# Kernel tuning notes

Measured on AMD Instinct MI355X. Metric: run time of the kernel, lower is better.

Reference implementation:

```python
import jax, jax.numpy as jnp
import numpy as np

BATCH, SEQ, H, P, HID, CHUNK = 2, 2048, 32, 64, 2048, 256
NORM_EPS = 1e-5


def setup_inputs() -> dict:
    key = jax.random.key(0)
    ks = jax.random.split(key, 10)
    f = lambda k, sh, sc=1.0: jax.random.normal(k, sh, jnp.float32) * sc
    return {
        "hidden_states_ab": f(ks[0], (BATCH, SEQ, HID), 0.02),
        "hidden_states_g": f(ks[1], (BATCH, SEQ, HID), 0.02),
        "q_states": f(ks[2], (BATCH, SEQ, H, P)),
        "k_states": f(ks[3], (BATCH, SEQ, H, P)),
        "v_states": f(ks[4], (BATCH, SEQ, H, P)),
        "dt_w": f(ks[5], (HID, H), 0.02),
        "dt_b": jnp.zeros((H,), jnp.float32),
        "g_w": f(ks[6], (HID, H), 0.02),
        "g_b": jnp.zeros((H,), jnp.float32),
        "A_log": jnp.log(jnp.arange(1, H + 1, dtype=jnp.float32)),
        "dt_bias": jnp.ones((H,), jnp.float32),
        "norm_weight": jnp.ones((H * P,), jnp.float32),
        "o_w": f(ks[7], (H, P, P), 0.02),
        "o_b": jnp.zeros((H, P), jnp.float32),
    }


def _l2norm(x, eps=1e-12):
    # torch F.normalize(p=2, dim=-1): x / max(||x||, eps)
    n = jnp.sqrt(jnp.sum(x * x, axis=-1, keepdims=True))
    return x / jnp.maximum(n, eps)


def _ssd(x, dt, A, Bm, Cm, chunk):
    # x: (b,s,h,p)  dt: (b,s,h) post-softplus  A: (h,)  Bm/Cm: (b,s,h,n)
    b, s, h, p = x.shape
    n = Bm.shape[-1]
    c = s // chunk
    rs = lambda t: t.reshape(b, c, chunk, *t.shape[2:])
    x, dt, Bm, Cm = rs(x), rs(dt), rs(Bm), rs(Cm)
    a = dt * A                         # (b,c,L,h) log-decay increments
    cum = jnp.cumsum(a, axis=2)        # (b,c,L,h)
    cumT = jnp.swapaxes(cum, 2, 3)     # (b,c,h,L)
    # intra-chunk (quadratic, causal) part
    diff = cumT[..., :, None] - cumT[..., None, :]          # (b,c,h,L,L)
    mask = jnp.tril(jnp.ones((chunk, chunk), bool))
    decay = jnp.exp(jnp.where(mask, diff, -jnp.inf))
    CB = jnp.einsum('bclhn,bcshn->bchls', Cm, Bm)
    scores = CB * decay * jnp.swapaxes(dt, 2, 3)[:, :, :, None, :]
    y = jnp.einsum('bchls,bcshp->bclhp', scores, x)
    # per-chunk states
    decay_last = jnp.exp(cumT[..., -1:] - cumT)             # (b,c,h,L)
    w = jnp.swapaxes(decay_last, 2, 3) * dt                 # (b,c,L,h)
    states = jnp.einsum('bclh,bclhn,bclhp->bchpn', w, Bm, x)
    # inter-chunk recurrence over c chunks
    chunk_decay = jnp.exp(cumT[..., -1])                    # (b,c,h)
    def step(Hs, inp):
        cd, st = inp
        return cd[..., None, None] * Hs + st, Hs
    H_last, H_prev = jax.lax.scan(
        step, jnp.zeros((b, h, p, n), x.dtype),
        (jnp.moveaxis(chunk_decay, 1, 0), jnp.moveaxis(states, 1, 0)))
    H_prev = jnp.moveaxis(H_prev, 0, 1)                     # (b,c,h,p,n)
    y = y + jnp.einsum('bclhn,bclh,bchpn->bclhp', Cm, jnp.exp(cum), H_prev)
    return y.reshape(b, s, h, p), H_last


def reference(hidden_states_ab, hidden_states_g, q_states, k_states, v_states,
              dt_w, dt_b, g_w, g_b, A_log, dt_bias, norm_weight, o_w, o_b):
    b, s, h, p = v_states.shape
    Cm = _l2norm(q_states)
    Bm = _l2norm(k_states)
    # dt_proj bias + mamba dt_bias, then softplus (dt_softplus=True)
    dt = jax.nn.softplus(hidden_states_ab @ dt_w + dt_b + dt_bias)   # (b,s,h)
    A = -jnp.exp(A_log)
    y, ssm_state = _ssd(v_states, dt, A, Bm, Cm, CHUNK)
    # gate: g_proj then repeat_interleave(head_dim) on last dim
    gate = jnp.repeat(hidden_states_g @ g_w + g_b, p, axis=-1)       # (b,s,h*p)
    # RMSNormGated, norm_before_gate=False: normalize(x * silu(z)) * weight
    y = y.reshape(b, s, h * p) * jax.nn.silu(gate)
    y = y * jax.lax.rsqrt(jnp.mean(y * y, axis=-1, keepdims=True) + NORM_EPS)
    y = y * norm_weight
    # GroupLinear o_proj: per-head (p -> p) linear
    out = jnp.einsum('bshp,hpq->bshq', y.reshape(b, s, h, p), o_w) + o_b
    return out.reshape(b, s, h * p)
```

## Files before the change

kernel.cpp:

```cpp
#include <hip/hip_runtime.h>
#include <math.h>

#define BATCH 2
#define SEQ   2048
#define NH    32
#define HID   2048
#define CHUNK 256
#define NCH   8
#define NBCH  (BATCH*NCH*NH)
#define PST   72
#define BK    256
#define APST  264
#define KSPLIT 4
#define KSEG  (HID / KSPLIT)

typedef __attribute__((ext_vector_type(4))) float f32x4;
typedef __attribute__((ext_vector_type(8))) short bf16x8;
typedef unsigned int uint;
typedef unsigned short ushort;

__device__ __forceinline__ float softplusf(float x) {
    return x > 20.f ? x : log1pf(expf(x));
}

__device__ __forceinline__ short f2bf(float f) {
    union { float f; uint u; } v; v.f = f;
    uint r = v.u + 0x7FFF + ((v.u >> 16) & 1);
    return (short)(r >> 16);
}
__device__ __forceinline__ float bf2f(ushort s) {
    union { uint u; float f; } v; v.u = ((uint)s) << 16; return v.f;
}
__device__ __forceinline__ uint packbf2(float lo, float hi) {
    return (uint)(ushort)f2bf(lo) | ((uint)(ushort)f2bf(hi) << 16);
}

struct BF8 { union { bf16x8 v; short s[8]; }; };

__device__ __forceinline__ bf16x8 load_cvt8(const float* p, float scale) {
    float4 a = *(const float4*)p;
    float4 b = *(const float4*)(p + 4);
    BF8 r;
    r.s[0]=f2bf(a.x*scale); r.s[1]=f2bf(a.y*scale); r.s[2]=f2bf(a.z*scale); r.s[3]=f2bf(a.w*scale);
    r.s[4]=f2bf(b.x*scale); r.s[5]=f2bf(b.y*scale); r.s[6]=f2bf(b.z*scale); r.s[7]=f2bf(b.w*scale);
    return r.v;
}

__device__ __forceinline__ bf16x8 cvt8(float4 a, float4 b, float s) {
    BF8 r;
    r.s[0]=f2bf(a.x*s); r.s[1]=f2bf(a.y*s); r.s[2]=f2bf(a.z*s); r.s[3]=f2bf(a.w*s);
    r.s[4]=f2bf(b.x*s); r.s[5]=f2bf(b.y*s); r.s[6]=f2bf(b.z*s); r.s[7]=f2bf(b.w*s);
    return r.v;
}

#define MFMA(a,b,c) __builtin_amdgcn_mfma_f32_16x16x32_bf16((a),(b),(c),0,0,0)

__global__ __launch_bounds__(256) void k_proj(
    const float* __restrict__ hs_ab, const float* __restrict__ hs_g,
    const float* __restrict__ dt_w, const float* __restrict__ g_w,
    const float* __restrict__ o_w,  const float* __restrict__ norm_w,
    float* __restrict__ part, short* __restrict__ nwWT)
{
    __shared__ __align__(16) short As[32 * APST];
    __shared__ __align__(16) short Bs[32 * APST];
    int blk = blockIdx.x;
    int t = threadIdx.x;

    if (blk >= 2 * KSPLIT * 128) {
        int h = blk - 2 * KSPLIT * 128;
        float* tile = (float*)As;
        {
            int p = t >> 2, q0 = (t & 3) * 16;
            const float* wp = o_w + (size_t)h * 4096 + p * 64 + q0;
            #pragma unroll
            for (int i = 0; i < 4; ++i)
                *(float4*)(tile + p * 64 + q0 + i * 4) = *(const float4*)(wp + i * 4);
        }
        __syncthreads();
        int q = t >> 2, p0 = (t & 3) * 16;
        uint us[8];
        #pragma unroll
        for (int j = 0; j < 8; ++j) {
            float lo = tile[(p0 + 2*j    ) * 64 + q] * norm_w[h * 64 + p0 + 2*j];
            float hi = tile[(p0 + 2*j + 1) * 64 + q] * norm_w[h * 64 + p0 + 2*j + 1];
            us[j] = packbf2(lo, hi);
        }
        uint* dst = (uint*)(nwWT + (size_t)h * 4096 + q * 64 + p0);
        *(uint4*)dst       = make_uint4(us[0], us[1], us[2], us[3]);
        *(uint4*)(dst + 4) = make_uint4(us[4], us[5], us[6], us[7]);
        return;
    }

    int ksp = blk >> 8;
    int rem = blk & 255;
    int which = rem >> 7;
    int rt = rem & 127;
    int r0 = rt * 32;
    const float* Am = which ? hs_g : hs_ab;
    const float* W  = which ? g_w  : dt_w;
    int w = t >> 6, lane = t & 63, quad = lane >> 4, l16 = lane & 15;
    int mh = w & 1, nh = w >> 1;

    f32x4 acc = (f32x4){0.f, 0.f, 0.f, 0.f};

    for (int kc = ksp * KSEG; kc < ksp * KSEG + KSEG; kc += BK) {
        __syncthreads();
        {
            int row = t >> 3, k0 = (t & 7) * 32;
            const float* src = Am + (size_t)(r0 + row) * HID + kc + k0;
            uint* dst = (uint*)(As + row * APST + k0);
            #pragma unroll
            for (int i = 0; i < 4; ++i) {
                float4 a = *(const float4*)(src + i * 8);
                float4 b = *(const float4*)(src + i * 8 + 4);
                dst[i*4+0] = packbf2(a.x, a.y); dst[i*4+1] = packbf2(a.z, a.w);
                dst[i*4+2] = packbf2(b.x, b.y); dst[i*4+3] = packbf2(b.z, b.w);
            }
        }
        if (t < 128) {
            int k2 = t * 2;
            const float* w0 = W + (size_t)(kc + k2) * NH;
            const float* w1 = w0 + NH;
            #pragma unroll
            for (int n = 0; n < 32; n += 4) {
                float4 a = *(const float4*)(w0 + n);
                float4 b = *(const float4*)(w1 + n);
                *((uint*)(Bs + (n+0) * APST + k2)) = packbf2(a.x, b.x);
                *((uint*)(Bs + (n+1) * APST + k2)) = packbf2(a.y, b.y);
                *((uint*)(Bs + (n+2) * APST + k2)) = packbf2(a.z, b.z);
                *((uint*)(Bs + (n+3) * APST + k2)) = packbf2(a.w, b.w);
            }
        }
        __syncthreads();
        #pragma unroll
        for (int ks = 0; ks < BK / 32; ++ks) {
            bf16x8 af = *(const bf16x8*)(As + (mh*16 + l16) * APST + ks*32 + quad*8);
            bf16x8 bf = *(const bf16x8*)(Bs + (nh*16 + l16) * APST + ks*32 + quad*8);
            acc = MFMA(af, bf, acc);
        }
    }

    int n = nh * 16 + l16;
    int Rb = r0 + mh * 16 + quad * 4;
    float* pd = part + ((size_t)(which * KSPLIT + ksp) * 4096 + Rb) * 32 + n;
    #pragma unroll
    for (int r = 0; r < 4; ++r)
        pd[r * 32] = acc[r];
}

__global__ __launch_bounds__(256) void k_cumsum(
    const float* __restrict__ part, const float* __restrict__ dt_b,
    const float* __restrict__ dt_bias, const float* __restrict__ A_log,
    float* __restrict__ cumc, float* __restrict__ wvc,
    float* __restrict__ dtc, float* __restrict__ cd)
{
    __shared__ float wsum[4];
    int bch = blockIdx.x;
    int h = bch & 31, c = (bch >> 5) & 7, b = bch >> 8;
    int t = threadIdx.x;
    int w = t >> 6, lane = t & 63;
    int rid = (b * SEQ + c * CHUNK + t) * 32 + h;
    float s = part[rid] + part[131072 + rid] + part[262144 + rid] + part[393216 + rid];
    float dt_l = softplusf(s + dt_b[h] + dt_bias[h]);
    float A = -expf(A_log[h]);
    float v = dt_l * A;
    #pragma unroll
    for (int off = 1; off < 64; off <<= 1) {
        float u = __shfl_up(v, off);
        if (lane >= off) v += u;
    }
    if (lane == 63) wsum[w] = v;
    __syncthreads();
    float pre = 0.f;
    #pragma unroll
    for (int i = 0; i < 3; ++i)
        if (i < w) pre += wsum[i];
    float cum = v + pre;
    float tot = wsum[0] + wsum[1] + wsum[2] + wsum[3];
    size_t o = (size_t)bch * CHUNK + t;
    cumc[o] = cum;
    wvc[o] = expf(tot - cum) * dt_l;
    dtc[o] = dt_l;
    if (t == 255) cd[bch] = expf(tot);
}

__global__ __launch_bounds__(256) void k_states(
    const float* __restrict__ kst, const float* __restrict__ vst,
    const float* __restrict__ wvc, float* __restrict__ sp)
{
    __shared__ __align__(16) float kS[64 * 64];
    __shared__ __align__(16) float xS[64 * 64];
    int blk = blockIdx.x;
    int half = blk & 1, bch = blk >> 1;
    int h = bch & 31, c = (bch >> 5) & 7, b = bch >> 8;
    int t = threadIdx.x;
    size_t rowbase = (size_t)b * SEQ + c * CHUNK + half * 128;
    int pg = (t & 15) * 4, ng = (t >> 4) * 4;
    float acc[4][4];
    #pragma unroll
    for (int i = 0; i < 4; ++i)
        #pragma unroll
        for (int j = 0; j < 4; ++j) acc[i][j] = 0.f;

    for (int tt = 0; tt < 2; ++tt) {
        int r0 = t >> 4;
        int c4 = (t & 15) * 4;
        #pragma unroll
        for (int i = 0; i < 4; ++i) {
            int row = r0 + i * 16;
            size_t grow = (rowbase + tt * 64 + row) * NH + h;
            float wv = wvc[(size_t)bch * CHUNK + half * 128 + tt * 64 + row];
            float4 kv = *(const float4*)(kst + grow * 64 + c4);
            float4 xv = *(const float4*)(vst + grow * 64 + c4);
            float ssq = kv.x*kv.x + kv.y*kv.y + kv.z*kv.z + kv.w*kv.w;
            ssq += __shfl_xor(ssq, 1); ssq += __shfl_xor(ssq, 2);
            ssq += __shfl_xor(ssq, 4); ssq += __shfl_xor(ssq, 8);
            float ib = 1.f / fmaxf(sqrtf(ssq), 1e-12f);
            *(float4*)(kS + row * 64 + c4) =
                make_float4(kv.x * ib, kv.y * ib, kv.z * ib, kv.w * ib);
            *(float4*)(xS + row * 64 + c4) =
                make_float4(xv.x * wv, xv.y * wv, xv.z * wv, xv.w * wv);
        }
        __syncthreads();
        for (int ll = 0; ll < 64; ++ll) {
            float4 x4 = *(const float4*)(xS + ll * 64 + pg);
            float4 k4 = *(const float4*)(kS + ll * 64 + ng);
            acc[0][0] += x4.x * k4.x; acc[0][1] += x4.x * k4.y;
            acc[0][2] += x4.x * k4.z; acc[0][3] += x4.x * k4.w;
            acc[1][0] += x4.y * k4.x; acc[1][1] += x4.y * k4.y;
            acc[1][2] += x4.y * k4.z; acc[1][3] += x4.y * k4.w;
            acc[2][0] += x4.z * k4.x; acc[2][1] += x4.z * k4.y;
            acc[2][2] += x4.z * k4.z; acc[2][3] += x4.z * k4.w;
            acc[3][0] += x4.w * k4.x; acc[3][1] += x4.w * k4.y;
            acc[3][2] += x4.w * k4.z; acc[3][3] += x4.w * k4.w;
        }
        __syncthreads();
    }
    size_t obase = (size_t)blk * 4096;
    #pragma unroll
    for (int i = 0; i < 4; ++i)
        *(float4*)(sp + obase + (pg + i) * 64 + ng) =
            make_float4(acc[i][0], acc[i][1], acc[i][2], acc[i][3]);
}

__global__ __launch_bounds__(256) void k_scan(
    const float* __restrict__ sp, const float* __restrict__ cd,
    float* __restrict__ Hp)
{
    size_t id = (size_t)blockIdx.x * 256 + threadIdx.x;
    size_t bh = id >> 12, pn = id & 4095;
    size_t b = bh >> 5, h = bh & 31;
    float carry = 0.f;
    for (int c = 0; c < NCH; ++c) {
        size_t bch = (b * NCH + c) * NH + h;
        float st = sp[(bch * 2) * 4096 + pn] + sp[(bch * 2 + 1) * 4096 + pn];
        Hp[bch * 4096 + pn] = carry;
        carry = cd[bch] * carry + st;
    }
}

__global__ __launch_bounds__(256, 2) void k_intra(
    const float* __restrict__ qst, const float* __restrict__ kst,
    const float* __restrict__ vst,
    const float* __restrict__ cumc, const float* __restrict__ dtc,
    const float* __restrict__ Hp,
    short* __restrict__ ygb)
{
    __shared__ __align__(16) short B_s[2][64 * PST];
    __shared__ __align__(16) short XT_s[2][64 * PST];
    __shared__ __align__(16) short P_s[4 * 32 * PST];
    __shared__ float sCum[256];
    __shared__ float sDt[256];

    int bch = blockIdx.x;
    int h = bch & 31, c = (bch >> 5) & 7, b = bch >> 8;
    int t = threadIdx.x;
    int w = t >> 6, lane = t & 63;
    int quad = lane >> 4, l16 = lane & 15;
    size_t rowbase = (size_t)b * SEQ + c * CHUNK;

    sCum[t] = cumc[(size_t)bch * CHUNK + t];
    sDt[t]  = dtc[(size_t)bch * CHUNK + t];

    int ssA = t >> 2, q4A = (t & 3) * 16;
    int ss2 = t & 31, p0 = (t >> 5) * 8;

    float4 kv[4], xa[2], xb[2];
    {
        size_t gK = (rowbase + ssA) * NH + h;
        const float4* kp = (const float4*)(kst + gK * 64 + q4A);
        kv[0] = kp[0]; kv[1] = kp[1]; kv[2] = kp[2]; kv[3] = kp[3];
        size_t g0 = (rowbase + 2 * ss2) * NH + h;
        const float* vp0 = vst + g0 * 64 + p0;
        const float* vp1 = vst + (g0 + NH) * 64 + p0;
        xa[0] = *(const float4*)vp0; xa[1] = *(const float4*)(vp0 + 4);
        xb[0] = *(const float4*)vp1; xb[1] = *(const float4*)(vp1 + 4);
    }

    bf16x8 cf[2][2][2];
    #pragma unroll
    for (int is = 0; is < 2; ++is) {
        int strip = is ? (7 - w) : w;
        #pragma unroll
        for (int lt = 0; lt < 2; ++lt) {
            int l = strip * 32 + lt * 16 + l16;
            size_t grow = (rowbase + l) * NH + h;
            const float* qp = qst + grow * 64 + quad * 8;
            float4 a  = *(const float4*)qp;
            float4 bq = *(const float4*)(qp + 4);
            float4 c2 = *(const float4*)(qp + 32);
            float4 d  = *(const float4*)(qp + 36);
            float ssq = a.x*a.x + a.y*a.y + a.z*a.z + a.w*a.w
                      + bq.x*bq.x + bq.y*bq.y + bq.z*bq.z + bq.w*bq.w
                      + c2.x*c2.x + c2.y*c2.y + c2.z*c2.z + c2.w*c2.w
                      + d.x*d.x + d.y*d.y + d.z*d.z + d.w*d.w;
            ssq += __shfl_xor(ssq, 16);
            ssq += __shfl_xor(ssq, 32);
            float ic = 1.f / fmaxf(sqrtf(ssq), 1e-12f);
            cf[is][lt][0] = cvt8(a, bq, ic);
            cf[is][lt][1] = cvt8(c2, d, ic);
        }
    }

    f32x4 acc[2][2][4];
    #pragma unroll
    for (int is = 0; is < 2; ++is)
        #pragma unroll
        for (int lt = 0; lt < 2; ++lt)
            #pragma unroll
            for (int pt = 0; pt < 4; ++pt)
                acc[is][lt][pt] = (f32x4){0.f, 0.f, 0.f, 0.f};

    {
        bf16x8 hf[4][2];
        #pragma unroll
        for (int pt = 0; pt < 4; ++pt) {
            const float* hp = Hp + (size_t)bch * 4096 + (pt * 16 + l16) * 64 + quad * 8;
            hf[pt][0] = load_cvt8(hp, 1.f);
            hf[pt][1] = load_cvt8(hp + 32, 1.f);
        }
        #pragma unroll
        for (int is = 0; is < 2; ++is)
            #pragma unroll
            for (int lt = 0; lt < 2; ++lt)
                #pragma unroll
                for (int pt = 0; pt < 4; ++pt) {
                    acc[is][lt][pt] = MFMA(cf[is][lt][0], hf[pt][0], acc[is][lt][pt]);
                    acc[is][lt][pt] = MFMA(cf[is][lt][1], hf[pt][1], acc[is][lt][pt]);
                }
    }
    __syncthreads();
    #pragma unroll
    for (int is = 0; is < 2; ++is) {
        int strip = is ? (7 - w) : w;
        #pragma unroll
        for (int lt = 0; lt < 2; ++lt) {
            float e[4];
            #pragma unroll
            for (int r = 0; r < 4; ++r)
                e[r] = __expf(sCum[strip * 32 + lt * 16 + quad * 4 + r]);
            #pragma unroll
            for (int pt = 0; pt < 4; ++pt)
                #pragma unroll
                for (int r = 0; r < 4; ++r)
                    acc[is][lt][pt][r] *= e[r];
        }
    }

    short* Pw = P_s + w * 32 * PST;

    #pragma unroll
    for (int st = 0; st < 4; ++st) {
        float4 kvN[4], xaN[2], xbN[2];
        if (st < 3) {
            size_t gK = (rowbase + (st + 1) * 64 + ssA) * NH + h;
            const float4* kp = (const float4*)(kst + gK * 64 + q4A);
            kvN[0] = kp[0]; kvN[1] = kp[1]; kvN[2] = kp[2]; kvN[3] = kp[3];
            size_t g0 = (rowbase + (st + 1) * 64 + 2 * ss2) * NH + h;
            const float* vp0 = vst + g0 * 64 + p0;
            const float* vp1 = vst + (g0 + NH) * 64 + p0;
            xaN[0] = *(const float4*)vp0; xaN[1] = *(const float4*)(vp0 + 4);
            xbN[0] = *(const float4*)vp1; xbN[1] = *(const float4*)(vp1 + 4);
        }

        short* Bb = B_s[st & 1];
        short* Xb = XT_s[st & 1];
        {
            float ssq = kv[0].x*kv[0].x + kv[0].y*kv[0].y + kv[0].z*kv[0].z + kv[0].w*kv[0].w
                      + kv[1].x*kv[1].x + kv[1].y*kv[1].y + kv[1].z*kv[1].z + kv[1].w*kv[1].w
                      + kv[2].x*kv[2].x + kv[2].y*kv[2].y + kv[2].z*kv[2].z + kv[2].w*kv[2].w
                      + kv[3].x*kv[3].x + kv[3].y*kv[3].y + kv[3].z*kv[3].z + kv[3].w*kv[3].w;
            ssq += __shfl_xor(ssq, 1);
            ssq += __shfl_xor(ssq, 2);
            float ib = 1.f / fmaxf(sqrtf(ssq), 1e-12f);
            uint u[8];
            u[0] = packbf2(kv[0].x * ib, kv[0].y * ib); u[1] = packbf2(kv[0].z * ib, kv[0].w * ib);
            u[2] = packbf2(kv[1].x * ib, kv[1].y * ib); u[3] = packbf2(kv[1].z * ib, kv[1].w * ib);
            u[4] = packbf2(kv[2].x * ib, kv[2].y * ib); u[5] = packbf2(kv[2].z * ib, kv[2].w * ib);
            u[6] = packbf2(kv[3].x * ib, kv[3].y * ib); u[7] = packbf2(kv[3].z * ib, kv[3].w * ib);
            uint* dst = (uint*)(Bb + ssA * PST + q4A);
            *(uint4*)dst = make_uint4(u[0], u[1], u[2], u[3]);
            *(uint4*)(dst + 4) = make_uint4(u[4], u[5], u[6], u[7]);
        }
        {
            float dt0 = sDt[st * 64 + 2 * ss2];
            float dt1 = sDt[st * 64 + 2 * ss2 + 1];
            float x0[8] = {xa[0].x, xa[0].y, xa[0].z, xa[0].w,
                           xa[1].x, xa[1].y, xa[1].z, xa[1].w};
            float x1[8] = {xb[0].x, xb[0].y, xb[0].z, xb[0].w,
                           xb[1].x, xb[1].y, xb[1].z, xb[1].w};
            uint* xt = (uint*)Xb;
            #pragma unroll
            for (int i = 0; i < 8; ++i)
                xt[(p0 + i) * (PST / 2) + ss2] = packbf2(x0[i] * dt0, x1[i] * dt1);
        }
        __syncthreads();

        bf16x8 xf[4][2];
        #pragma unroll
        for (int pt = 0; pt < 4; ++pt) {
            #pragma unroll
            for (int ks = 0; ks < 2; ++ks)
                xf[pt][ks] = *(const bf16x8*)(Xb + (pt * 16 + l16) * PST + ks * 32 + quad * 8);
        }

        #pragma unroll
        for (int is = 0; is < 2; ++is) {
            int strip = is ? (7 - w) : w;
            int L0 = strip * 32;
            if (L0 + 31 < st * 64) continue;

            #pragma unroll
            for (int lt = 0; lt < 2; ++lt) {
                int Lt = L0 + lt * 16;
                float cl = sCum[Lt + l16];
                int lrow = lt * 16 + l16;
                #pragma unroll
                for (int mt = 0; mt < 4; ++mt) {
                    int S0 = st * 64 + mt * 16;
                    uint* pdst = (uint*)(Pw + lrow * PST + mt * 16 + quad * 4);
                    if (S0 > Lt + 15) {
                        *(uint2*)pdst = make_uint2(0u, 0u);
                        continue;
                    }
                    f32x4 sa = (f32x4){0.f, 0.f, 0.f, 0.f};
                    bf16x8 af0 = *(const bf16x8*)(Bb + (mt * 16 + l16) * PST + quad * 8);
                    bf16x8 af1 = *(const bf16x8*)(Bb + (mt * 16 + l16) * PST + 32 + quad * 8);
                    sa = MFMA(af0, cf[is][lt][0], sa);
                    sa = MFMA(af1, cf[is][lt][1], sa);
                    float vals[4];
                    #pragma unroll
                    for (int r = 0; r < 4; ++r) {
                        int s = S0 + quad * 4 + r;
                        float v = sa[r] * __expf(cl - sCum[s]);
                        vals[r] = (Lt + l16 >= s) ? v : 0.f;
                    }
                    *(uint2*)pdst = make_uint2(packbf2(vals[0], vals[1]),
                                               packbf2(vals[2], vals[3]));
                }
            }
            #pragma unroll
            for (int lt = 0; lt < 2; ++lt) {
                int Lmax = L0 + lt * 16 + 15;
                #pragma unroll
                for (int ks = 0; ks < 2; ++ks) {
                    if (st * 64 + ks * 32 > Lmax) continue;
                    bf16x8 af = *(const bf16x8*)(Pw + (lt * 16 + l16) * PST + ks * 32 + quad * 8);
                    #pragma unroll
                    for (int pt = 0; pt < 4; ++pt)
                        acc[is][lt][pt] = MFMA(af, xf[pt][ks], acc[is][lt][pt]);
                }
            }
        }

        if (st < 3) {
            kv[0] = kvN[0]; kv[1] = kvN[1]; kv[2] = kvN[2]; kv[3] = kvN[3];
            xa[0] = xaN[0]; xa[1] = xaN[1];
            xb[0] = xbN[0]; xb[1] = xbN[1];
        }
    }

    #pragma unroll
    for (int is = 0; is < 2; ++is) {
        int strip = is ? (7 - w) : w;
        #pragma unroll
        for (int lt = 0; lt < 2; ++lt)
            #pragma unroll
            for (int pt = 0; pt < 4; ++pt)
                #pragma unroll
                for (int r = 0; r < 4; ++r) {
                    int l = strip * 32 + lt * 16 + quad * 4 + r;
                    int p = pt * 16 + l16;
                    ygb[((rowbase + l) * NH + h) * 64 + p] = f2bf(acc[is][lt][pt][r]);
                }
    }
}

__global__ __launch_bounds__(256) void k_out(
    const short* __restrict__ ygb, const float* __restrict__ part,
    const float* __restrict__ g_b, const short* __restrict__ nwWT,
    const float* __restrict__ o_b, float* __restrict__ out)
{
    __shared__ __align__(16) short yS[16 * 1024];
    __shared__ float silS[16 * 32];
    __shared__ float scaleS[16];
    int blk = blockIdx.x;
    int half = blk & 1, rt = blk >> 1;
    int r0 = rt * 16;
    int t = threadIdx.x;
    int w = t >> 6, lane = t & 63, quad = lane >> 4, l16 = lane & 15;

    const float* gpart = part + 4 * 131072;
    #pragma unroll
    for (int ii = 0; ii < 2; ++ii) {
        int idx = t + ii * 256;
        int rr = idx >> 5, hh = idx & 31;
        int rid = (r0 + rr) * 32 + hh;
        float g = gpart[rid] + gpart[131072 + rid] + gpart[262144 + rid]
                + gpart[393216 + rid] + g_b[hh];
        silS[idx] = g / (1.f + expf(-g));
    }
    __syncthreads();

    int r = t >> 4, cl = t & 15;
    const char* yrow = (const char*)(ygb + (size_t)(r0 + r) * 2048);
    float ssq = 0.f;
    #pragma unroll
    for (int i = 0; i < 16; ++i) {
        int cb = i * 256 + cl * 16;
        uint4 u = *(const uint4*)(yrow + cb);
        float s = silS[r * 32 + (cb >> 7)];
        float v0 = bf2f((ushort)(u.x & 0xFFFF)) * s, v1 = bf2f((ushort)(u.x >> 16)) * s;
        float v2 = bf2f((ushort)(u.y & 0xFFFF)) * s, v3 = bf2f((ushort)(u.y >> 16)) * s;
        float v4 = bf2f((ushort)(u.z & 0xFFFF)) * s, v5 = bf2f((ushort)(u.z >> 16)) * s;
        float v6 = bf2f((ushort)(u.w & 0xFFFF)) * s, v7 = bf2f((ushort)(u.w >> 16)) * s;
        ssq += v0*v0 + v1*v1 + v2*v2 + v3*v3 + v4*v4 + v5*v5 + v6*v6 + v7*v7;
        if ((cb >> 11) == half) {
            int cbl = cb & 2047;
            *(uint4*)((char*)yS + r * 2048 + (cbl ^ ((r & 7) << 4))) = u;
        }
    }
    ssq += __shfl_xor(ssq, 1); ssq += __shfl_xor(ssq, 2);
    ssq += __shfl_xor(ssq, 4); ssq += __shfl_xor(ssq, 8);
    if (cl == 0) scaleS[r] = rsqrtf(ssq / 2048.f + 1e-5f);
    __syncthreads();

    #pragma unroll
    for (int hh = 0; hh < 4; ++hh) {
        int h = half * 16 + w * 4 + hh;
        int hl = h & 15;
        const short* wb = nwWT + (size_t)h * 4096;
        bf16x8 bfr[4][2];
        #pragma unroll
        for (int nt = 0; nt < 4; ++nt)
            #pragma unroll
            for (int ks = 0; ks < 2; ++ks)
                bfr[nt][ks] = *(const bf16x8*)(wb + (nt * 16 + l16) * 64 + ks * 32 + quad * 8);
        bf16x8 af[2];
        #pragma unroll
        for (int ks = 0; ks < 2; ++ks) {
            int cbl = hl * 128 + ks * 64 + quad * 16;
            af[ks] = *(const bf16x8*)((const char*)yS + l16 * 2048 + (cbl ^ ((l16 & 7) << 4)));
        }
        f32x4 acc[4];
        #pragma unroll
        for (int nt = 0; nt < 4; ++nt) acc[nt] = (f32x4){0.f, 0.f, 0.f, 0.f};
        #pragma unroll
        for (int ks = 0; ks < 2; ++ks)
            #pragma unroll
            for (int nt = 0; nt < 4; ++nt)
                acc[nt] = MFMA(af[ks], bfr[nt][ks], acc[nt]);
        #pragma unroll
        for (int nt = 0; nt < 4; ++nt) {
            float bv = o_b[h * 64 + nt * 16 + l16];
            #pragma unroll
            for (int rr = 0; rr < 4; ++rr) {
                int row = quad * 4 + rr;
                float o = acc[nt][rr] * silS[row * 32 + h] * scaleS[row] + bv;
                out[(size_t)(r0 + row) * 2048 + h * 64 + nt * 16 + l16] = o;
            }
        }
    }
}

extern "C" void kernel_launch(void* const* d_in, const int* in_sizes, int n_in,
                              void* d_out, int out_size, void* d_ws, size_t ws_size,
                              hipStream_t stream) {
    const float* hs_ab   = (const float*)d_in[0];
    const float* hs_g    = (const float*)d_in[1];
    const float* qst     = (const float*)d_in[2];
    const float* kst     = (const float*)d_in[3];
    const float* vst     = (const float*)d_in[4];
    const float* dt_w    = (const float*)d_in[5];
    const float* dt_b    = (const float*)d_in[6];
    const float* g_w     = (const float*)d_in[7];
    const float* g_b     = (const float*)d_in[8];
    const float* A_log   = (const float*)d_in[9];
    const float* dt_bias = (const float*)d_in[10];
    const float* norm_w  = (const float*)d_in[11];
    const float* o_w     = (const float*)d_in[12];
    const float* o_b     = (const float*)d_in[13];
    float* out = (float*)d_out;

    float* ws = (float*)d_ws;
    size_t off = 0;
    float* part   = ws + off; off += (size_t)2 * KSPLIT * 4096 * 32;
    float* cumc   = ws + off; off += (size_t)NBCH * CHUNK;
    float* wvc    = ws + off; off += (size_t)NBCH * CHUNK;
    float* dtc    = ws + off; off += (size_t)NBCH * CHUNK;
    float* cd_ws  = ws + off; off += (size_t)NBCH;
    float* sp     = ws + off; off += (size_t)NBCH * 2 * 4096;
    float* Hp     = ws + off; off += (size_t)NBCH * 4096;
    short* nwWT   = (short*)(ws + off); off += (size_t)NH * 64 * 64 / 2;

    short* ygb = (short*)sp;

    k_proj<<<2 * KSPLIT * (BATCH * SEQ / 32) + NH, 256, 0, stream>>>(
        hs_ab, hs_g, dt_w, g_w, o_w, norm_w, part, nwWT);
    k_cumsum<<<NBCH, 256, 0, stream>>>(part, dt_b, dt_bias, A_log,
                                       cumc, wvc, dtc, cd_ws);
    k_states<<<NBCH * 2, 256, 0, stream>>>(kst, vst, wvc, sp);
    k_scan<<<BATCH * NH * 4096 / 256, 256, 0, stream>>>(sp, cd_ws, Hp);
    k_intra<<<NBCH, 256, 0, stream>>>(qst, kst, vst, cumc, dtc, Hp, ygb);
    k_out<<<2 * (BATCH * SEQ / 16), 256, 0, stream>>>(ygb, part, g_b, nwWT, o_b, out);
}
```

Measured before the change: 268.3 us.

## Split intra-chunk kernel into two half-blocks per chunk for more parallelism

Each (batch,chunk,head) is now handled by two blocks, one per half of the 256 output rows. The block with the upper rows iterates all 4 key stages, the block with the lower rows only 2. The per-warp register state halves, launch bounds rise to 4 blocks/SM, and B/X shared buffers are single-buffered with an extra barrier per stage. The aim is to double the grid (512 to 1024 blocks) and raise occupancy. In exchange, K/V and Hp loads for early stages are duplicated across the two blocks, and the two blocks get unequal amounts of work.

```diff
diff --git a/kernel.cpp b/kernel.cpp
--- a/kernel.cpp
+++ b/kernel.cpp
@@ -259,24 +259,28 @@
     }
 }
 
-__global__ __launch_bounds__(256, 2) void k_intra(
+__global__ __launch_bounds__(256, 4) void k_intra(
     const float* __restrict__ qst, const float* __restrict__ kst,
     const float* __restrict__ vst,
     const float* __restrict__ cumc, const float* __restrict__ dtc,
     const float* __restrict__ Hp,
     short* __restrict__ ygb)
 {
-    __shared__ __align__(16) short B_s[2][64 * PST];
-    __shared__ __align__(16) short XT_s[2][64 * PST];
+    __shared__ __align__(16) short B_s[64 * PST];
+    __shared__ __align__(16) short XT_s[64 * PST];
     __shared__ __align__(16) short P_s[4 * 32 * PST];
     __shared__ float sCum[256];
     __shared__ float sDt[256];
 
-    int bch = blockIdx.x;
+    int blk = blockIdx.x;
+    int half = (blk < NBCH) ? 1 : 0;
+    int bch = blk & (NBCH - 1);
     int h = bch & 31, c = (bch >> 5) & 7, b = bch >> 8;
     int t = threadIdx.x;
     int w = t >> 6, lane = t & 63;
     int quad = lane >> 4, l16 = lane & 15;
+    int strip = half * 4 + w;
+    int nst = half ? 4 : 2;
     size_t rowbase = (size_t)b * SEQ + c * CHUNK;
 
     sCum[t] = cumc[(size_t)bch * CHUNK + t];
@@ -297,39 +301,33 @@
         xb[0] = *(const float4*)vp1; xb[1] = *(const float4*)(vp1 + 4);
     }
 
-    bf16x8 cf[2][2][2];
-    #pragma unroll
-    for (int is = 0; is < 2; ++is) {
-        int strip = is ? (7 - w) : w;
-        #pragma unroll
-        for (int lt = 0; lt < 2; ++lt) {
-            int l = strip * 32 + lt * 16 + l16;
-            size_t grow = (rowbase + l) * NH + h;
-            const float* qp = qst + grow * 64 + quad * 8;
-            float4 a  = *(const float4*)qp;
-            float4 bq = *(const float4*)(qp + 4);
-            float4 c2 = *(const float4*)(qp + 32);
-            float4 d  = *(const float4*)(qp + 36);
-            float ssq = a.x*a.x + a.y*a.y + a.z*a.z + a.w*a.w
-                      + bq.x*bq.x + bq.y*bq.y + bq.z*bq.z + bq.w*bq.w
-                      + c2.x*c2.x + c2.y*c2.y + c2.z*c2.z + c2.w*c2.w
-                      + d.x*d.x + d.y*d.y + d.z*d.z + d.w*d.w;
-            ssq += __shfl_xor(ssq, 16);
-            ssq += __shfl_xor(ssq, 32);
-            float ic = 1.f / fmaxf(sqrtf(ssq), 1e-12f);
-            cf[is][lt][0] = cvt8(a, bq, ic);
-            cf[is][lt][1] = cvt8(c2, d, ic);
-        }
-    }
-
-    f32x4 acc[2][2][4];
-    #pragma unroll
-    for (int is = 0; is < 2; ++is)
-        #pragma unroll
-        for (int lt = 0; lt < 2; ++lt)
-            #pragma unroll
-            for (int pt = 0; pt < 4; ++pt)
-                acc[is][lt][pt] = (f32x4){0.f, 0.f, 0.f, 0.f};
+    bf16x8 cf[2][2];
+    #pragma unroll
+    for (int lt = 0; lt < 2; ++lt) {
+        int l = strip * 32 + lt * 16 + l16;
+        size_t grow = (rowbase + l) * NH + h;
+        const float* qp = qst + grow * 64 + quad * 8;
+        float4 a  = *(const float4*)qp;
+        float4 bq = *(const float4*)(qp + 4);
+        float4 c2 = *(const float4*)(qp + 32);
+        float4 d  = *(const float4*)(qp + 36);
+        float ssq = a.x*a.x + a.y*a.y + a.z*a.z + a.w*a.w
+                  + bq.x*bq.x + bq.y*bq.y + bq.z*bq.z + bq.w*bq.w
+                  + c2.x*c2.x + c2.y*c2.y + c2.z*c2.z + c2.w*c2.w
+                  + d.x*d.x + d.y*d.y + d.z*d.z + d.w*d.w;
+        ssq += __shfl_xor(ssq, 16);
+        ssq += __shfl_xor(ssq, 32);
+        float ic = 1.f / fmaxf(sqrtf(ssq), 1e-12f);
+        cf[lt][0] = cvt8(a, bq, ic);
+        cf[lt][1] = cvt8(c2, d, ic);
+    }
+
+    f32x4 acc[2][4];
+    #pragma unroll
+    for (int lt = 0; lt < 2; ++lt)
+        #pragma unroll
+        for (int pt = 0; pt < 4; ++pt)
+            acc[lt][pt] = (f32x4){0.f, 0.f, 0.f, 0.f};
 
     {
         bf16x8 hf[4][2];
@@ -340,39 +338,33 @@
             hf[pt][1] = load_cvt8(hp + 32, 1.f);
         }
         #pragma unroll
-        for (int is = 0; is < 2; ++is)
-            #pragma unroll
-            for (int lt = 0; lt < 2; ++lt)
-                #pragma unroll
-                for (int pt = 0; pt < 4; ++pt) {
-                    acc[is][lt][pt] = MFMA(cf[is][lt][0], hf[pt][0], acc[is][lt][pt]);
-                    acc[is][lt][pt] = MFMA(cf[is][lt][1], hf[pt][1], acc[is][lt][pt]);
-                }
+        for (int lt = 0; lt < 2; ++lt)
+            #pragma unroll
+            for (int pt = 0; pt < 4; ++pt) {
+                acc[lt][pt] = MFMA(cf[lt][0], hf[pt][0], acc[lt][pt]);
+                acc[lt][pt] = MFMA(cf[lt][1], hf[pt][1], acc[lt][pt]);
+            }
     }
     __syncthreads();
     #pragma unroll
-    for (int is = 0; is < 2; ++is) {
-        int strip = is ? (7 - w) : w;
-        #pragma unroll
-        for (int lt = 0; lt < 2; ++lt) {
-            float e[4];
+    for (int lt = 0; lt < 2; ++lt) {
+        float e[4];
+        #pragma unroll
+        for (int r = 0; r < 4; ++r)
+            e[r] = __expf(sCum[strip * 32 + lt * 16 + quad * 4 + r]);
+        #pragma unroll
+        for (int pt = 0; pt < 4; ++pt)
             #pragma unroll
             for (int r = 0; r < 4; ++r)
-                e[r] = __expf(sCum[strip * 32 + lt * 16 + quad * 4 + r]);
-            #pragma unroll
-            for (int pt = 0; pt < 4; ++pt)
-                #pragma unroll
-                for (int r = 0; r < 4; ++r)
-                    acc[is][lt][pt][r] *= e[r];
-        }
+                acc[lt][pt][r] *= e[r];
     }
 
     short* Pw = P_s + w * 32 * PST;
 
-    #pragma unroll
-    for (int st = 0; st < 4; ++st) {
+    for (int st = 0; st < nst; ++st) {
         float4 kvN[4], xaN[2], xbN[2];
-        if (st < 3) {
+        bool pf = (st + 1 < nst);
+        if (pf) {
             size_t gK = (rowbase + (st + 1) * 64 + ssA) * NH + h;
             const float4* kp = (const float4*)(kst + gK * 64 + q4A);
             kvN[0] = kp[0]; kvN[1] = kp[1]; kvN[2] = kp[2]; kvN[3] = kp[3];
@@ -383,8 +375,6 @@
             xbN[0] = *(const float4*)vp1; xbN[1] = *(const float4*)(vp1 + 4);
         }
 
-        short* Bb = B_s[st & 1];
-        short* Xb = XT_s[st & 1];
         {
             float ssq = kv[0].x*kv[0].x + kv[0].y*kv[0].y + kv[0].z*kv[0].z + kv[0].w*kv[0].w
                       + kv[1].x*kv[1].x + kv[1].y*kv[1].y + kv[1].z*kv[1].z + kv[1].w*kv[1].w
@@ -398,7 +388,7 @@
             u[2] = packbf2(kv[1].x * ib, kv[1].y * ib); u[3] = packbf2(kv[1].z * ib, kv[1].w * ib);
             u[4] = packbf2(kv[2].x * ib, kv[2].y * ib); u[5] = packbf2(kv[2].z * ib, kv[2].w * ib);
             u[6] = packbf2(kv[3].x * ib, kv[3].y * ib); u[7] = packbf2(kv[3].z * ib, kv[3].w * ib);
-            uint* dst = (uint*)(Bb + ssA * PST + q4A);
+            uint* dst = (uint*)(B_s + ssA * PST + q4A);
             *(uint4*)dst = make_uint4(u[0], u[1], u[2], u[3]);
             *(uint4*)(dst + 4) = make_uint4(u[4], u[5], u[6], u[7]);
         }
@@ -409,30 +399,25 @@
                            xa[1].x, xa[1].y, xa[1].z, xa[1].w};
             float x1[8] = {xb[0].x, xb[0].y, xb[0].z, xb[0].w,
                            xb[1].x, xb[1].y, xb[1].z, xb[1].w};
-            uint* xt = (uint*)Xb;
+            uint* xt = (uint*)XT_s;
             #pragma unroll
             for (int i = 0; i < 8; ++i)
                 xt[(p0 + i) * (PST / 2) + ss2] = packbf2(x0[i] * dt0, x1[i] * dt1);
         }
         __syncthreads();
 
-        bf16x8 xf[4][2];
-        #pragma unroll
-        for (int pt = 0; pt < 4; ++pt) {
-            #pragma unroll
-            for (int ks = 0; ks < 2; ++ks)
-                xf[pt][ks] = *(const bf16x8*)(Xb + (pt * 16 + l16) * PST + ks * 32 + quad * 8);
-        }
-
-        #pragma unroll
-        for (int is = 0; is < 2; ++is) {
-            int strip = is ? (7 - w) : w;
-            int L0 = strip * 32;
-            if (L0 + 31 < st * 64) continue;
+        if (strip * 32 + 31 >= st * 64) {
+            bf16x8 xf[4][2];
+            #pragma unroll
+            for (int pt = 0; pt < 4; ++pt) {
+                #pragma unroll
+                for (int ks = 0; ks < 2; ++ks)
+                    xf[pt][ks] = *(const bf16x8*)(XT_s + (pt * 16 + l16) * PST + ks * 32 + quad * 8);
+            }
 
             #pragma unroll
             for (int lt = 0; lt < 2; ++lt) {
-                int Lt = L0 + lt * 16;
+                int Lt = strip * 32 + lt * 16;
                 float cl = sCum[Lt + l16];
                 int lrow = lt * 16 + l16;
                 #pragma unroll
@@ -444,10 +429,10 @@
                         continue;
                     }
                     f32x4 sa = (f32x4){0.f, 0.f, 0.f, 0.f};
-                    bf16x8 af0 = *(const bf16x8*)(Bb + (mt * 16 + l16) * PST + quad * 8);
-                    bf16x8 af1 = *(const bf16x8*)(Bb + (mt * 16 + l16) * PST + 32 + quad * 8);
-                    sa = MFMA(af0, cf[is][lt][0], sa);
-                    sa = MFMA(af1, cf[is][lt][1], sa);
+                    bf16x8 af0 = *(const bf16x8*)(B_s + (mt * 16 + l16) * PST + quad * 8);
+                    bf16x8 af1 = *(const bf16x8*)(B_s + (mt * 16 + l16) * PST + 32 + quad * 8);
+                    sa = MFMA(af0, cf[lt][0], sa);
+                    sa = MFMA(af1, cf[lt][1], sa);
                     float vals[4];
                     #pragma unroll
                     for (int r = 0; r < 4; ++r) {
@@ -461,19 +446,20 @@
             }
             #pragma unroll
             for (int lt = 0; lt < 2; ++lt) {
-                int Lmax = L0 + lt * 16 + 15;
+                int Lmax = strip * 32 + lt * 16 + 15;
                 #pragma unroll
                 for (int ks = 0; ks < 2; ++ks) {
                     if (st * 64 + ks * 32 > Lmax) continue;
                     bf16x8 af = *(const bf16x8*)(Pw + (lt * 16 + l16) * PST + ks * 32 + quad * 8);
                     #pragma unroll
                     for (int pt = 0; pt < 4; ++pt)
-                        acc[is][lt][pt] = MFMA(af, xf[pt][ks], acc[is][lt][pt]);
+                        acc[lt][pt] = MFMA(af, xf[pt][ks], acc[lt][pt]);
                 }
             }
         }
-
-        if (st < 3) {
+        __syncthreads();
+
+        if (pf) {
             kv[0] = kvN[0]; kv[1] = kvN[1]; kv[2] = kvN[2]; kv[3] = kvN[3];
             xa[0] = xaN[0]; xa[1] = xaN[1];
             xb[0] = xbN[0]; xb[1] = xbN[1];
@@ -481,19 +467,15 @@
     }
 
     #pragma unroll
-    for (int is = 0; is < 2; ++is) {
-        int strip = is ? (7 - w) : w;
-        #pragma unroll
-        for (int lt = 0; lt < 2; ++lt)
-            #pragma unroll
-            for (int pt = 0; pt < 4; ++pt)
-                #pragma unroll
-                for (int r = 0; r < 4; ++r) {
-                    int l = strip * 32 + lt * 16 + quad * 4 + r;
-                    int p = pt * 16 + l16;
-                    ygb[((rowbase + l) * NH + h) * 64 + p] = f2bf(acc[is][lt][pt][r]);
-                }
-    }
+    for (int lt = 0; lt < 2; ++lt)
+        #pragma unroll
+        for (int pt = 0; pt < 4; ++pt)
+            #pragma unroll
+            for (int r = 0; r < 4; ++r) {
+                int l = strip * 32 + lt * 16 + quad * 4 + r;
+                int p = pt * 16 + l16;
+                ygb[((rowbase + l) * NH + h) * 64 + p] = f2bf(acc[lt][pt][r]);
+            }
 }
 
 __global__ __launch_bounds__(256) void k_out(
@@ -621,6 +603,6 @@
                                        cumc, wvc, dtc, cd_ws);
     k_states<<<NBCH * 2, 256, 0, stream>>>(kst, vst, wvc, sp);
     k_scan<<<BATCH * NH * 4096 / 256, 256, 0, stream>>>(sp, cd_ws, Hp);
-    k_intra<<<NBCH, 256, 0, stream>>>(qst, kst, vst, cumc, dtc, Hp, ygb);
+    k_intra<<<NBCH * 2, 256, 0, stream>>>(qst, kst, vst, cumc, dtc, Hp, ygb);
     k_out<<<2 * (BATCH * SEQ / 16), 256, 0, stream>>>(ygb, part, g_b, nwWT, o_b, out);
 }
```

New measurement: 348.6 us. +29.9%, slower.
